# Kernel optimization log

Hardware: AMD Instinct MI355X
Metric: run time of the kernel (lower is better)

## Reference

```python
import jax, jax.numpy as jnp
import numpy as np

B, L, M, D = 8, 2048, 2048, 256


def setup_inputs() -> dict:
    key = jax.random.key(0)
    k1, k2, k3, k4, k5 = jax.random.split(key, 5)
    inp = jax.random.normal(k1, (B, L, D), dtype=jnp.float32)
    mem = jax.random.normal(k2, (B, M, D), dtype=jnp.float32)
    mask = jnp.ones((B, M), dtype=jnp.float32)
    # Learned parameters (Linear(D, 1, bias=False) -> weight vector of shape [D])
    w_input = jax.random.normal(k3, (D,), dtype=jnp.float32) / np.sqrt(D)
    w_memory = jax.random.normal(k4, (D,), dtype=jnp.float32) / np.sqrt(D)
    dot_scale = jax.random.uniform(k5, (D,), dtype=jnp.float32, minval=0.0, maxval=1.0 / np.sqrt(D))
    return {"input": inp, "memory": mem, "mask": mask,
            "w_input": w_input, "w_memory": w_memory, "dot_scale": dot_scale}


def reference(input, memory, mask, w_input, w_memory, dot_scale):
    # dropout with p=0.0 / eval mode -> identity
    input_dot = jnp.einsum('bld,d->bl', input, w_input)[:, :, None]      # [B, L, 1]
    memory_dot = jnp.einsum('bmd,d->bm', memory, w_memory)[:, None, :]   # [B, 1, M]
    cross_dot = jnp.einsum('bld,bmd->blm', input * dot_scale, memory)    # [B, L, M]
    att = input_dot + memory_dot + cross_dot                             # [B, L, M]
    att = att - 1e30 * (1.0 - mask[:, None, :])
    weight_one = jax.nn.softmax(att, axis=-1)                            # [B, L, M]
    output_one = jnp.einsum('blm,bmd->bld', weight_one, memory)          # [B, L, D]
    weight_two = jax.nn.softmax(jnp.max(att, axis=-1), axis=-1)[:, None, :]  # [B, 1, L]
    output_two = jnp.einsum('bol,bld->bod', weight_two, input)           # [B, 1, D]
    return jnp.concatenate(
        [input, output_one, input * output_one, output_two * output_one], axis=-1)
```

## Files before the change

kernel.cpp:

```cpp
#include <hip/hip_runtime.h>
#include <hip/hip_bf16.h>


typedef __bf16 bf16_t;
typedef bf16_t bf16x4 __attribute__((ext_vector_type(4)));
typedef bf16_t bf16x8 __attribute__((ext_vector_type(8)));
typedef float  f32x16 __attribute__((ext_vector_type(16)));

#define NB 8
#define NL 2048
#define NM 2048
#define ND 256
#define OUTW 1024
#define MT 32
#define MH 1024
#define NIT 32
#define LT 128
#define MEMT_X0 8388608u
#define FLASH_LDS 73728

__device__ __forceinline__ unsigned omap(unsigned x) {
    return ((x >> 10) << 12) | (x & 1023u);
}

__device__ __forceinline__ void dma16(const void* g, void* l) {
    __builtin_amdgcn_global_load_lds(
        (const __attribute__((address_space(1))) unsigned int*)g,
        (__attribute__((address_space(3))) unsigned int*)l, 16, 0, 0);
}

__global__ __launch_bounds__(256) void idot_kernel(
    const float* __restrict__ input, const float* __restrict__ w_input,
    float* __restrict__ ws_idot)
{
    int row  = blockIdx.x * 4 + (threadIdx.x >> 6);
    int lane = threadIdx.x & 63;
    float4 v  = *(const float4*)(input + (size_t)row * ND + lane * 4);
    float4 wv = *(const float4*)(w_input + lane * 4);
    float s = v.x * wv.x + v.y * wv.y + v.z * wv.z + v.w * wv.w;
    #pragma unroll
    for (int off = 1; off < 64; off <<= 1) s += __shfl_xor(s, off, 64);
    if (lane == 0) ws_idot[row] = s;
}

__global__ __launch_bounds__(256) void prep_kernel(
    const float* __restrict__ memory, const float* __restrict__ mask,
    const float* __restrict__ w_memory,
    float* __restrict__ ws_mbias, char* __restrict__ outc)
{
    __shared__ __align__(16) bf16_t lds[32 * 256];

    int b  = blockIdx.x >> 6;
    int mc = blockIdx.x & 63;
    int t  = threadIdx.x, w = t >> 6, lane = t & 63;

    float4 wv = *(const float4*)(w_memory + lane * 4);

    #pragma unroll
    for (int it = 0; it < 8; ++it) {
        int rloc = it * 4 + w;
        int row  = b * NM + mc * 32 + rloc;
        float4 v = *(const float4*)(memory + (size_t)row * ND + lane * 4);
        float s = v.x * wv.x + v.y * wv.y + v.z * wv.z + v.w * wv.w;
        #pragma unroll
        for (int off = 1; off < 64; off <<= 1) s += __shfl_xor(s, off, 64);
        if (lane == 0) ws_mbias[row] = s - 1e30f * (1.0f - mask[row]);
        bf16x4 bv;
        bv[0] = (bf16_t)v.x; bv[1] = (bf16_t)v.y;
        bv[2] = (bf16_t)v.z; bv[3] = (bf16_t)v.w;
        unsigned x = 2u * ((unsigned)row * ND + lane * 4);
        *(bf16x4*)(outc + omap(x)) = bv;
        *(bf16x4*)(&lds[rloc * 256 + lane * 4]) = bv;
    }
    __syncthreads();
    int d = t;
    #pragma unroll
    for (int mc4 = 0; mc4 < 4; ++mc4) {
        bf16x8 pk;
        #pragma unroll
        for (int j = 0; j < 8; ++j) pk[j] = lds[(mc4 * 8 + j) * 256 + d];
        unsigned x = MEMT_X0 +
            2u * ((((unsigned)(b * 256 + mc * 4 + mc4)) * ND + d) * 8);
        *(bf16x8*)(outc + omap(x)) = pk;
    }
}

__global__ __launch_bounds__(256, 1) void flash_kernel(
    const float* __restrict__ input, const float* __restrict__ dot_scale,
    const float* __restrict__ ws_mbias, const char* __restrict__ outc,
    float* __restrict__ out, float* __restrict__ ws_l, float* __restrict__ ws_m)
{
    extern __shared__ __align__(16) char smem[];

    int bid = blockIdx.x;
    int half = bid & 1, b = (bid >> 1) & 7, lt = bid >> 4;
    int l0 = lt * LT;
    int m_base = half * MH;
    int t = threadIdx.x, w = t >> 6, lane = t & 63;
    int c = lane & 31, h = lane >> 5;

    const float* qrow = input + (size_t)(b * NL + l0 + w * 32 + c) * ND;
    bf16x8 qf[16];
    #pragma unroll
    for (int ks = 0; ks < 16; ++ks) {
        int d0 = ks * 16 + h * 8;
        float4 a0 = *(const float4*)(qrow + d0);
        float4 a1 = *(const float4*)(qrow + d0 + 4);
        float4 s0 = *(const float4*)(dot_scale + d0);
        float4 s1 = *(const float4*)(dot_scale + d0 + 4);
        qf[ks][0] = (bf16_t)(a0.x * s0.x); qf[ks][1] = (bf16_t)(a0.y * s0.y);
        qf[ks][2] = (bf16_t)(a0.z * s0.z); qf[ks][3] = (bf16_t)(a0.w * s0.w);
        qf[ks][4] = (bf16_t)(a1.x * s1.x); qf[ks][5] = (bf16_t)(a1.y * s1.y);
        qf[ks][6] = (bf16_t)(a1.z * s1.z); qf[ks][7] = (bf16_t)(a1.w * s1.w);
    }

    unsigned xk = 2u * (((unsigned)(b * NM + m_base + c)) * ND + h * 8);
    const char* kg = outc + omap(xk);
    unsigned xv = MEMT_X0 +
        2u * ((((unsigned)(b * 256 + (m_base >> 3) + h)) * ND + c) * 8);
    const char* vg = outc + omap(xv);

    char* buf0 = smem;
    char* buf1 = smem + 32768;

    #pragma unroll
    for (int j = 0; j < 4; ++j) {
        int i = 4 * w + j;
        int ks = i >> 3, dt = i & 7;
        dma16(kg + i * 32, buf0 + i * 1024);
        dma16(vg + ks * 32768 + (dt >> 1) * 4096 + (dt & 1) * 512,
              buf0 + 16384 + i * 1024);
    }
    kg += 65536; vg += 65536;

    f32x16 oaccT[8];
    #pragma unroll
    for (int i = 0; i < 8; ++i)
        #pragma unroll
        for (int r = 0; r < 16; ++r) oaccT[i][r] = 0.f;
    float lsum = 0.f, mmax = -3e38f;

    const float* mb_base = ws_mbias + b * NM;
    bf16_t* pfw = (bf16_t*)(smem + 65536 + w * 2048);

    #pragma unroll 1
    for (int it = 0; it < NIT; ++it) {
        int m0 = m_base + it * MT;
        asm volatile("s_waitcnt vmcnt(0)" ::: "memory");
        __syncthreads();
        const char* cb = (it & 1) ? buf1 : buf0;
        char* nb = (it & 1) ? buf0 : buf1;
        const bf16_t* kb = (const bf16_t*)cb;
        const bf16_t* vb = (const bf16_t*)(cb + 16384);
        if (it + 1 < NIT) {
            #pragma unroll
            for (int j = 0; j < 4; ++j) {
                int i = 4 * w + j;
                int ks = i >> 3, dt = i & 7;
                dma16(kg + i * 32, nb + i * 1024);
                dma16(vg + ks * 32768 + (dt >> 1) * 4096 + (dt & 1) * 512,
                      nb + 16384 + i * 1024);
            }
            kg += 65536; vg += 65536;
        }
        float mb[16];
        #pragma unroll
        for (int r = 0; r < 16; ++r)
            mb[r] = mb_base[m0 + ((r & 3) + 8 * (r >> 2) + 4 * h)];
        f32x16 Sa, Sb;
        #pragma unroll
        for (int r = 0; r < 16; ++r) { Sa[r] = 0.f; Sb[r] = 0.f; }
        #pragma unroll
        for (int ks = 0; ks < 16; ks += 2) {
            bf16x8 k0 = *(const bf16x8*)(kb + ks * 512 + lane * 8);
            bf16x8 k1 = *(const bf16x8*)(kb + (ks + 1) * 512 + lane * 8);
            Sa = __builtin_amdgcn_mfma_f32_32x32x16_bf16(k0, qf[ks], Sa, 0, 0, 0);
            Sb = __builtin_amdgcn_mfma_f32_32x32x16_bf16(k1, qf[ks + 1], Sb, 0, 0, 0);
        }
        #pragma unroll
        for (int j2 = 0; j2 < 4; ++j2) {
            bf16x4 pk;
            #pragma unroll
            for (int q = 0; q < 4; ++q) {
                int r = j2 * 4 + q;
                float v = Sa[r] + Sb[r] + mb[r];
                mmax = fmaxf(mmax, v);
                float e = __expf(v);
                lsum += e;
                pk[q] = (bf16_t)e;
            }
            *(bf16x4*)(pfw + j2 * 256 + c * 8 + h * 4) = pk;
        }
        asm volatile("s_waitcnt lgkmcnt(0)" ::: "memory");
        #pragma unroll
        for (int ks = 0; ks < 2; ++ks) {
            bf16x8 pb = *(const bf16x8*)(pfw + ks * 512 + lane * 8);
            #pragma unroll
            for (int dt = 0; dt < 8; ++dt) {
                bf16x8 vv = *(const bf16x8*)(vb + (ks * 8 + dt) * 512 + lane * 8);
                oaccT[dt] = __builtin_amdgcn_mfma_f32_32x32x16_bf16(vv, pb, oaccT[dt], 0, 0, 0);
            }
        }
    }

    mmax = fmaxf(mmax, __shfl_xor(mmax, 32, 64));
    lsum += __shfl_xor(lsum, 32, 64);
    if (lane < 32) {
        int row = b * NL + l0 + w * 32 + lane;
        ws_l[half * (NB * NL) + row] = lsum;
        ws_m[half * (NB * NL) + row] = mmax;
    }
    float* patch = (float*)(smem + w * 4352);
    float* oseg = out + (size_t)(b * NL + l0 + w * 32) * OUTW + ND * (1 + half);
    #pragma unroll
    for (int dt = 0; dt < 8; ++dt) {
        asm volatile("s_waitcnt lgkmcnt(0)" ::: "memory");
        #pragma unroll
        for (int r = 0; r < 16; ++r)
            patch[((r & 3) + 8 * (r >> 2) + 4 * h) * 33 + c] = oaccT[dt][r];
        asm volatile("s_waitcnt lgkmcnt(0)" ::: "memory");
        #pragma unroll
        for (int rr = 0; rr < 16; ++rr) {
            float val = patch[c * 33 + rr * 2 + h];
            oseg[(size_t)(rr * 2 + h) * OUTW + dt * 32 + c] = val;
        }
    }
}

__global__ __launch_bounds__(256) void o2_kernel(
    const float* __restrict__ input, const float* __restrict__ ws_idot,
    const float* __restrict__ ws_m, float* __restrict__ ws_num,
    float* __restrict__ ws_den)
{
    int b = blockIdx.x >> 4, slice = blockIdx.x & 15;
    int t = threadIdx.x;
    int lgrp = t >> 6, d4 = (t & 63) * 4;
    float4 acc = {0.f, 0.f, 0.f, 0.f};
    float esum = 0.f;
    for (int i = 0; i < 32; ++i) {
        int row = b * NL + slice * 128 + lgrp * 32 + i;
        float e = __expf(ws_idot[row] + fmaxf(ws_m[row], ws_m[NB * NL + row]));
        float4 v = *(const float4*)(input + (size_t)row * ND + d4);
        acc.x += e * v.x; acc.y += e * v.y;
        acc.z += e * v.z; acc.w += e * v.w;
        esum += e;
    }
    float* dst = ws_num + b * ND + d4;
    atomicAdd(dst + 0, acc.x); atomicAdd(dst + 1, acc.y);
    atomicAdd(dst + 2, acc.z); atomicAdd(dst + 3, acc.w);
    if ((t & 63) == 0) atomicAdd(ws_den + b, esum);
}

__global__ __launch_bounds__(256) void assembly_kernel(
    const float* __restrict__ input, const float* __restrict__ ws_num,
    const float* __restrict__ ws_den, const float* __restrict__ ws_l,
    float* __restrict__ out)
{
    size_t tid = (size_t)blockIdx.x * 256 + threadIdx.x;
    size_t row = tid >> 6;
    int d = (int)(tid & 63) * 4;
    int b = (int)(row >> 11);
    float inv  = 1.0f / (ws_l[row] + ws_l[NB * NL + row]);
    float dinv = 1.0f / ws_den[b];
    float* po = out + row * OUTW;
    float4 in = *(const float4*)(input + row * ND + d);
    float4 pa = *(const float4*)(po + ND + d);
    float4 pb = *(const float4*)(po + 2 * ND + d);
    float4 nu = *(const float4*)(ws_num + b * ND + d);
    float4 o1;
    o1.x = (pa.x + pb.x) * inv; o1.y = (pa.y + pb.y) * inv;
    o1.z = (pa.z + pb.z) * inv; o1.w = (pa.w + pb.w) * inv;
    float4 o2v;
    o2v.x = nu.x * dinv; o2v.y = nu.y * dinv;
    o2v.z = nu.z * dinv; o2v.w = nu.w * dinv;
    *(float4*)(po + d) = in;
    *(float4*)(po + ND + d) = o1;
    float4 q;
    q.x = in.x * o1.x; q.y = in.y * o1.y; q.z = in.z * o1.z; q.w = in.w * o1.w;
    *(float4*)(po + 2 * ND + d) = q;
    float4 r;
    r.x = o2v.x * o1.x; r.y = o2v.y * o1.y; r.z = o2v.z * o1.z; r.w = o2v.w * o1.w;
    *(float4*)(po + 3 * ND + d) = r;
}

extern "C" void kernel_launch(void* const* d_in, const int* in_sizes, int n_in,
                              void* d_out, int out_size, void* d_ws, size_t ws_size,
                              hipStream_t stream) {
    const float* input     = (const float*)d_in[0];
    const float* memory    = (const float*)d_in[1];
    const float* mask      = (const float*)d_in[2];
    const float* w_input   = (const float*)d_in[3];
    const float* w_memory  = (const float*)d_in[4];
    const float* dot_scale = (const float*)d_in[5];
    float* out = (float*)d_out;
    char* outc = (char*)d_out;
    float* ws  = (float*)d_ws;

    float* ws_idot  = ws;
    float* ws_mbias = ws + 16384;
    float* ws_l     = ws + 32768;
    float* ws_m     = ws + 65536;
    float* ws_num   = ws + 98304;
    float* ws_den   = ws + 100352;

    idot_kernel<<<4096, 256, 0, stream>>>(input, w_input, ws_idot);
    prep_kernel<<<512, 256, 0, stream>>>(memory, mask, w_memory, ws_mbias, outc);
    flash_kernel<<<256, 256, FLASH_LDS, stream>>>(input, dot_scale, ws_mbias,
                                                  outc, out, ws_l, ws_m);
    hipMemsetAsync(ws_num, 0, (NB * ND + NB) * sizeof(float), stream);
    o2_kernel<<<128, 256, 0, stream>>>(input, ws_idot, ws_m, ws_num, ws_den);
    assembly_kernel<<<4096, 256, 0, stream>>>(input, ws_num, ws_den, ws_l, out);
}
```

Measured before the change: 205.4 us.

## Split flash kernel M-range across two wave groups with LDS reduction

The flash kernel now runs 512 threads per block: two groups of four waves each handle a different 32-column slice of each 64-wide memory tile, then reduce partial output accumulators and softmax statistics through LDS at the end. This doubles the waves available to hide MFMA and DMA latency on a grid of only 256 blocks, at the cost of twice the LDS per block and an extra reduction pass. The mask bias is now loaded once per lane and broadcast with shuffles instead of 16 scalar loads. Separately, the memset is folded into prep_kernel, and o2_kernel uses more blocks with an in-block LDS reduction before its atomics.

```diff
diff --git a/kernel.cpp b/kernel.cpp
--- a/kernel.cpp
+++ b/kernel.cpp
@@ -12,12 +12,12 @@
 #define NM 2048
 #define ND 256
 #define OUTW 1024
-#define MT 32
+#define MT 64
 #define MH 1024
-#define NIT 32
+#define NIT 16
 #define LT 128
 #define MEMT_X0 8388608u
-#define FLASH_LDS 73728
+#define FLASH_LDS 147456
 
 __device__ __forceinline__ unsigned omap(unsigned x) {
     return ((x >> 10) << 12) | (x & 1023u);
@@ -46,13 +46,18 @@
 __global__ __launch_bounds__(256) void prep_kernel(
     const float* __restrict__ memory, const float* __restrict__ mask,
     const float* __restrict__ w_memory,
-    float* __restrict__ ws_mbias, char* __restrict__ outc)
+    float* __restrict__ ws_mbias, float* __restrict__ ws_numden,
+    char* __restrict__ outc)
 {
     __shared__ __align__(16) bf16_t lds[32 * 256];
 
     int b  = blockIdx.x >> 6;
     int mc = blockIdx.x & 63;
     int t  = threadIdx.x, w = t >> 6, lane = t & 63;
+
+    if (blockIdx.x == 0) {
+        for (int k = t; k < 2056; k += 256) ws_numden[k] = 0.f;
+    }
 
     float4 wv = *(const float4*)(w_memory + lane * 4);
 
@@ -85,7 +90,7 @@
     }
 }
 
-__global__ __launch_bounds__(256, 1) void flash_kernel(
+__global__ __launch_bounds__(512, 2) void flash_kernel(
     const float* __restrict__ input, const float* __restrict__ dot_scale,
     const float* __restrict__ ws_mbias, const char* __restrict__ outc,
     float* __restrict__ out, float* __restrict__ ws_l, float* __restrict__ ws_m)
@@ -97,9 +102,10 @@
     int l0 = lt * LT;
     int m_base = half * MH;
     int t = threadIdx.x, w = t >> 6, lane = t & 63;
+    int gw = w & 3, grp = w >> 2;
     int c = lane & 31, h = lane >> 5;
 
-    const float* qrow = input + (size_t)(b * NL + l0 + w * 32 + c) * ND;
+    const float* qrow = input + (size_t)(b * NL + l0 + gw * 32 + c) * ND;
     bf16x8 qf[16];
     #pragma unroll
     for (int ks = 0; ks < 16; ++ks) {
@@ -114,24 +120,27 @@
         qf[ks][6] = (bf16_t)(a1.z * s1.z); qf[ks][7] = (bf16_t)(a1.w * s1.w);
     }
 
-    unsigned xk = 2u * (((unsigned)(b * NM + m_base + c)) * ND + h * 8);
+    unsigned xk = 2u * (((unsigned)(b * NM + m_base + grp * 32 + c)) * ND + h * 8);
     const char* kg = outc + omap(xk);
     unsigned xv = MEMT_X0 +
-        2u * ((((unsigned)(b * 256 + (m_base >> 3) + h)) * ND + c) * 8);
+        2u * ((((unsigned)(b * 256 + (m_base >> 3) + grp * 4 + h)) * ND + c) * 8);
     const char* vg = outc + omap(xv);
 
     char* buf0 = smem;
-    char* buf1 = smem + 32768;
-
-    #pragma unroll
-    for (int j = 0; j < 4; ++j) {
-        int i = 4 * w + j;
-        int ks = i >> 3, dt = i & 7;
-        dma16(kg + i * 32, buf0 + i * 1024);
-        dma16(vg + ks * 32768 + (dt >> 1) * 4096 + (dt & 1) * 512,
-              buf0 + 16384 + i * 1024);
-    }
-    kg += 65536; vg += 65536;
+    char* buf1 = smem + 65536;
+
+    #define STAGE(nbuf) do {                                                  \
+        _Pragma("unroll")                                                     \
+        for (int j = 0; j < 4; ++j) {                                         \
+            int i = gw * 4 + j;                                               \
+            int ks = i >> 3, dt = i & 7;                                      \
+            dma16(kg + i * 32, (nbuf) + grp * 16384 + i * 1024);              \
+            dma16(vg + ks * 32768 + (dt >> 1) * 4096 + (dt & 1) * 512,        \
+                  (nbuf) + 32768 + grp * 16384 + i * 1024);                   \
+        }                                                                     \
+        kg += 131072; vg += 131072; } while (0)
+
+    STAGE(buf0);
 
     f32x16 oaccT[8];
     #pragma unroll
@@ -141,41 +150,28 @@
     float lsum = 0.f, mmax = -3e38f;
 
     const float* mb_base = ws_mbias + b * NM;
-    bf16_t* pfw = (bf16_t*)(smem + 65536 + w * 2048);
+    bf16_t* pfw = (bf16_t*)(smem + 131072 + w * 2048);
 
     #pragma unroll 1
     for (int it = 0; it < NIT; ++it) {
-        int m0 = m_base + it * MT;
+        int m0 = m_base + it * MT + grp * 32;
         asm volatile("s_waitcnt vmcnt(0)" ::: "memory");
         __syncthreads();
         const char* cb = (it & 1) ? buf1 : buf0;
         char* nb = (it & 1) ? buf0 : buf1;
-        const bf16_t* kb = (const bf16_t*)cb;
-        const bf16_t* vb = (const bf16_t*)(cb + 16384);
+        const bf16_t* kb = (const bf16_t*)(cb + grp * 16384);
+        const bf16_t* vb = (const bf16_t*)(cb + 32768 + grp * 16384);
         if (it + 1 < NIT) {
-            #pragma unroll
-            for (int j = 0; j < 4; ++j) {
-                int i = 4 * w + j;
-                int ks = i >> 3, dt = i & 7;
-                dma16(kg + i * 32, nb + i * 1024);
-                dma16(vg + ks * 32768 + (dt >> 1) * 4096 + (dt & 1) * 512,
-                      nb + 16384 + i * 1024);
-            }
-            kg += 65536; vg += 65536;
-        }
-        float mb[16];
-        #pragma unroll
-        for (int r = 0; r < 16; ++r)
-            mb[r] = mb_base[m0 + ((r & 3) + 8 * (r >> 2) + 4 * h)];
-        f32x16 Sa, Sb;
-        #pragma unroll
-        for (int r = 0; r < 16; ++r) { Sa[r] = 0.f; Sb[r] = 0.f; }
-        #pragma unroll
-        for (int ks = 0; ks < 16; ks += 2) {
+            STAGE(nb);
+        }
+        float mv = mb_base[m0 + c];
+        f32x16 S;
+        #pragma unroll
+        for (int r = 0; r < 16; ++r) S[r] = 0.f;
+        #pragma unroll
+        for (int ks = 0; ks < 16; ++ks) {
             bf16x8 k0 = *(const bf16x8*)(kb + ks * 512 + lane * 8);
-            bf16x8 k1 = *(const bf16x8*)(kb + (ks + 1) * 512 + lane * 8);
-            Sa = __builtin_amdgcn_mfma_f32_32x32x16_bf16(k0, qf[ks], Sa, 0, 0, 0);
-            Sb = __builtin_amdgcn_mfma_f32_32x32x16_bf16(k1, qf[ks + 1], Sb, 0, 0, 0);
+            S = __builtin_amdgcn_mfma_f32_32x32x16_bf16(k0, qf[ks], S, 0, 0, 0);
         }
         #pragma unroll
         for (int j2 = 0; j2 < 4; ++j2) {
@@ -183,7 +179,7 @@
             #pragma unroll
             for (int q = 0; q < 4; ++q) {
                 int r = j2 * 4 + q;
-                float v = Sa[r] + Sb[r] + mb[r];
+                float v = S[r] + __shfl(mv, (r & 3) + 8 * (r >> 2) + 4 * h, 64);
                 mmax = fmaxf(mmax, v);
                 float e = __expf(v);
                 lsum += e;
@@ -202,27 +198,64 @@
             }
         }
     }
-
-    mmax = fmaxf(mmax, __shfl_xor(mmax, 32, 64));
-    lsum += __shfl_xor(lsum, 32, 64);
-    if (lane < 32) {
-        int row = b * NL + l0 + w * 32 + lane;
-        ws_l[half * (NB * NL) + row] = lsum;
-        ws_m[half * (NB * NL) + row] = mmax;
-    }
-    float* patch = (float*)(smem + w * 4352);
-    float* oseg = out + (size_t)(b * NL + l0 + w * 32) * OUTW + ND * (1 + half);
-    #pragma unroll
-    for (int dt = 0; dt < 8; ++dt) {
-        asm volatile("s_waitcnt lgkmcnt(0)" ::: "memory");
-        #pragma unroll
-        for (int r = 0; r < 16; ++r)
-            patch[((r & 3) + 8 * (r >> 2) + 4 * h) * 33 + c] = oaccT[dt][r];
-        asm volatile("s_waitcnt lgkmcnt(0)" ::: "memory");
-        #pragma unroll
-        for (int rr = 0; rr < 16; ++rr) {
-            float val = patch[c * 33 + rr * 2 + h];
-            oseg[(size_t)(rr * 2 + h) * OUTW + dt * 32 + c] = val;
+    #undef STAGE
+
+    __syncthreads();
+    if (grp == 1) {
+        float* dst = (float*)(smem + gw * 32768);
+        #pragma unroll
+        for (int dt = 0; dt < 8; ++dt) {
+            #pragma unroll
+            for (int q = 0; q < 4; ++q) {
+                float4 v4;
+                v4.x = oaccT[dt][q * 4 + 0]; v4.y = oaccT[dt][q * 4 + 1];
+                v4.z = oaccT[dt][q * 4 + 2]; v4.w = oaccT[dt][q * 4 + 3];
+                *(float4*)(dst + dt * 1024 + q * 256 + lane * 4) = v4;
+            }
+        }
+        float* aux = (float*)(smem + 131072 + gw * 2048);
+        aux[lane] = lsum;
+        aux[64 + lane] = mmax;
+    }
+    __syncthreads();
+    if (grp == 0) {
+        const float* src = (const float*)(smem + gw * 32768);
+        #pragma unroll
+        for (int dt = 0; dt < 8; ++dt) {
+            #pragma unroll
+            for (int q = 0; q < 4; ++q) {
+                float4 v4 = *(const float4*)(src + dt * 1024 + q * 256 + lane * 4);
+                oaccT[dt][q * 4 + 0] += v4.x; oaccT[dt][q * 4 + 1] += v4.y;
+                oaccT[dt][q * 4 + 2] += v4.z; oaccT[dt][q * 4 + 3] += v4.w;
+            }
+        }
+        const float* aux = (const float*)(smem + 131072 + gw * 2048);
+        lsum += aux[lane];
+        mmax = fmaxf(mmax, aux[64 + lane]);
+    }
+    __syncthreads();
+    if (grp == 0) {
+        mmax = fmaxf(mmax, __shfl_xor(mmax, 32, 64));
+        lsum += __shfl_xor(lsum, 32, 64);
+        if (lane < 32) {
+            int row = b * NL + l0 + gw * 32 + lane;
+            ws_l[half * (NB * NL) + row] = lsum;
+            ws_m[half * (NB * NL) + row] = mmax;
+        }
+        float* patch = (float*)(smem + gw * 4352);
+        float* oseg = out + (size_t)(b * NL + l0 + gw * 32) * OUTW + ND * (1 + half);
+        #pragma unroll
+        for (int dt = 0; dt < 8; ++dt) {
+            asm volatile("s_waitcnt lgkmcnt(0)" ::: "memory");
+            #pragma unroll
+            for (int r = 0; r < 16; ++r)
+                patch[((r & 3) + 8 * (r >> 2) + 4 * h) * 33 + c] = oaccT[dt][r];
+            asm volatile("s_waitcnt lgkmcnt(0)" ::: "memory");
+            #pragma unroll
+            for (int rr = 0; rr < 16; ++rr) {
+                float val = patch[c * 33 + rr * 2 + h];
+                oseg[(size_t)(rr * 2 + h) * OUTW + dt * 32 + c] = val;
+            }
         }
     }
 }
@@ -232,22 +265,30 @@
     const float* __restrict__ ws_m, float* __restrict__ ws_num,
     float* __restrict__ ws_den)
 {
-    int b = blockIdx.x >> 4, slice = blockIdx.x & 15;
+    __shared__ float4 red[256];
+    int b = blockIdx.x >> 5, slice = blockIdx.x & 31;
     int t = threadIdx.x;
     int lgrp = t >> 6, d4 = (t & 63) * 4;
     float4 acc = {0.f, 0.f, 0.f, 0.f};
     float esum = 0.f;
-    for (int i = 0; i < 32; ++i) {
-        int row = b * NL + slice * 128 + lgrp * 32 + i;
+    for (int i = 0; i < 16; ++i) {
+        int row = b * NL + slice * 64 + lgrp * 16 + i;
         float e = __expf(ws_idot[row] + fmaxf(ws_m[row], ws_m[NB * NL + row]));
         float4 v = *(const float4*)(input + (size_t)row * ND + d4);
         acc.x += e * v.x; acc.y += e * v.y;
         acc.z += e * v.z; acc.w += e * v.w;
         esum += e;
     }
-    float* dst = ws_num + b * ND + d4;
-    atomicAdd(dst + 0, acc.x); atomicAdd(dst + 1, acc.y);
-    atomicAdd(dst + 2, acc.z); atomicAdd(dst + 3, acc.w);
+    red[t] = acc;
+    __syncthreads();
+    if (t < 64) {
+        float4 a0 = red[t], a1 = red[t + 64], a2 = red[t + 128], a3 = red[t + 192];
+        float* dst = ws_num + b * ND + t * 4;
+        atomicAdd(dst + 0, a0.x + a1.x + a2.x + a3.x);
+        atomicAdd(dst + 1, a0.y + a1.y + a2.y + a3.y);
+        atomicAdd(dst + 2, a0.z + a1.z + a2.z + a3.z);
+        atomicAdd(dst + 3, a0.w + a1.w + a2.w + a3.w);
+    }
     if ((t & 63) == 0) atomicAdd(ws_den + b, esum);
 }
 
@@ -304,10 +345,10 @@
     float* ws_den   = ws + 100352;
 
     idot_kernel<<<4096, 256, 0, stream>>>(input, w_input, ws_idot);
-    prep_kernel<<<512, 256, 0, stream>>>(memory, mask, w_memory, ws_mbias, outc);
-    flash_kernel<<<256, 256, FLASH_LDS, stream>>>(input, dot_scale, ws_mbias,
+    prep_kernel<<<512, 256, 0, stream>>>(memory, mask, w_memory, ws_mbias,
+                                         ws_num, outc);
+    flash_kernel<<<256, 512, FLASH_LDS, stream>>>(input, dot_scale, ws_mbias,
                                                   outc, out, ws_l, ws_m);
-    hipMemsetAsync(ws_num, 0, (NB * ND + NB) * sizeof(float), stream);
-    o2_kernel<<<128, 256, 0, stream>>>(input, ws_idot, ws_m, ws_num, ws_den);
+    o2_kernel<<<256, 256, 0, stream>>>(input, ws_idot, ws_m, ws_num, ws_den);
     assembly_kernel<<<4096, 256, 0, stream>>>(input, ws_num, ws_den, ws_l, out);
 }
```

Result: faster. 199.5 us (-2.8%).
